# Kernel optimization log

Measured on AMD Instinct MI355X. Metric: run time of the kernel, lower is better.

Reference implementation:

```python
import jax, jax.numpy as jnp
import numpy as np

N = 524288   # sparse points
C = 64       # io channels
AC = 128     # attn channels
H = 8        # heads
PS = 64      # patch size
HID = 256    # mlp hidden (mlp_ratio=2)
HD = AC // H # head dim
EPS = 1e-5


def _ln(x):
    mu = x.mean(-1, keepdims=True)
    v = x.var(-1, keepdims=True)
    return (x - mu) / jnp.sqrt(v + EPS)


def setup_inputs() -> dict:
    key = jax.random.key(0)
    ks = jax.random.split(key, 12)
    def w(k, shape, fan_in):
        return jax.random.normal(k, shape, jnp.float32) * (1.0 / np.sqrt(fan_in))
    return {
        "feats": jax.random.normal(ks[0], (N, C), jnp.float32),
        "w_pre": w(ks[1], (C, AC), C),    "b_pre": jnp.zeros((AC,), jnp.float32),
        "g1": jnp.ones((AC,), jnp.float32), "b1": jnp.zeros((AC,), jnp.float32),
        "w_qkv": w(ks[2], (AC, 3 * AC), AC), "b_qkv": jnp.zeros((3 * AC,), jnp.float32),
        "w_proj": w(ks[3], (AC, AC), AC), "b_proj": jnp.zeros((AC,), jnp.float32),
        "g2": jnp.ones((AC,), jnp.float32), "b2": jnp.zeros((AC,), jnp.float32),
        "w_m1": w(ks[4], (AC, HID), AC),  "b_m1": jnp.zeros((HID,), jnp.float32),
        "w_m2": w(ks[5], (HID, AC), HID), "b_m2": jnp.zeros((AC,), jnp.float32),
        "w_post": w(ks[6], (AC, C), AC),  "b_post": jnp.zeros((C,), jnp.float32),
    }


def reference(feats, w_pre, b_pre, g1, b1, w_qkv, b_qkv, w_proj, b_proj,
              g2, b2, w_m1, b_m1, w_m2, b_m2, w_post, b_post):
    # pre_proj: 1x1 sparse conv == pointwise linear on [N, C]
    x2 = feats @ w_pre + b_pre                            # [N, AC]
    # norm1 -> patch attention
    n1 = _ln(x2) * g1 + b1
    P = N // PS
    qkv = (n1 @ w_qkv + b_qkv).reshape(P, PS, 3, H, HD)   # patches of 64 pts
    q, k, v = qkv[:, :, 0], qkv[:, :, 1], qkv[:, :, 2]    # [P, PS, H, HD]
    scale = HD ** -0.5
    att = jnp.einsum('pqhd,pkhd->phqk', q, k) * scale     # [P, H, PS, PS]
    att = jax.nn.softmax(att, axis=-1)
    o = jnp.einsum('phqk,pkhd->pqhd', att, v).reshape(N, AC)
    h = o @ w_proj + b_proj
    x2 = x2 + h                                           # residual 1
    # norm2 -> pointwise MLP (1x1 conv -> GELU -> 1x1 conv)
    n2 = _ln(x2) * g2 + b2
    h2 = jax.nn.gelu(n2 @ w_m1 + b_m1, approximate=False) @ w_m2 + b_m2
    x2 = x2 + h2                                          # residual 2
    return x2 @ w_post + b_post                           # post_proj [N, C]
```

## Files before the change

### kernel.cpp

```cpp
#include <hip/hip_runtime.h>
#include <hip/hip_bf16.h>
#include <math.h>


typedef __bf16 bf16;
typedef __bf16 bf16x8 __attribute__((ext_vector_type(8)));
typedef __bf16 bf16x4 __attribute__((ext_vector_type(4)));
typedef float  f32x4  __attribute__((ext_vector_type(4)));

#define MFMA16(a, b, c) __builtin_amdgcn_mfma_f32_16x16x32_bf16((a), (b), (c), 0, 0, 0)

constexpr int OFF_PRE  = 0;
constexpr int OFF_QKV  = 8192;
constexpr int OFF_PROJ = 57344;
constexpr int OFF_M1   = 73728;
constexpr int OFF_M2   = 106496;
constexpr int OFF_POST = 139264;

template <int W>
__device__ __forceinline__ int swz(int row, int col) {
    constexpr int CH = W >> 3;
    constexpr int M  = (CH - 1) < 15 ? (CH - 1) : 15;
    const int c = (col >> 3) ^ (row & M);
    return row * W + c * 8 + (col & 7);
}

__device__ __forceinline__ bf16x8 zero8() {
    bf16x8 z;
#pragma unroll
    for (int j = 0; j < 8; ++j) z[j] = (bf16)0.0f;
    return z;
}

__device__ __forceinline__ void st4(bf16* p, const f32x4 v) {
    bf16x4 o;
#pragma unroll
    for (int r = 0; r < 4; ++r) o[r] = (bf16)v[r];
    *(bf16x4*)p = o;
}

__device__ __forceinline__ float gelu_f(float x) {
    const float u = 0.79788456f * x * (1.0f + 0.044715f * x * x);
    const float e = __builtin_amdgcn_exp2f(u * 2.8853900817779268f);
    return x - x * __builtin_amdgcn_rcpf(e + 1.0f);
}

__global__ void pack_all(const float* __restrict__ w_pre,
                         const float* __restrict__ w_qkv,
                         const float* __restrict__ w_proj,
                         const float* __restrict__ w_m1,
                         const float* __restrict__ w_m2,
                         const float* __restrict__ w_post,
                         bf16* __restrict__ dst) {
    const int t = blockIdx.x;
    const float* src;
    int Ncol, KT, off, t0;
    if (t < 16)       { src = w_pre;  Ncol = 128; KT = 2; off = OFF_PRE;  t0 = 0; }
    else if (t < 112) { src = w_qkv;  Ncol = 384; KT = 4; off = OFF_QKV;  t0 = 16; }
    else if (t < 144) { src = w_proj; Ncol = 128; KT = 4; off = OFF_PROJ; t0 = 112; }
    else if (t < 208) { src = w_m1;   Ncol = 256; KT = 4; off = OFF_M1;   t0 = 144; }
    else if (t < 272) { src = w_m2;   Ncol = 128; KT = 8; off = OFF_M2;   t0 = 208; }
    else              { src = w_post; Ncol = 64;  KT = 4; off = OFF_POST; t0 = 272; }
    const int tile = t - t0;
    const int lane = threadIdx.x;
    const int mt = tile / KT, kt = tile - mt * KT;
    const int n  = mt * 16 + (lane & 15);
    const int k0 = kt * 32 + (lane >> 4) * 8;
    bf16x8 v;
#pragma unroll
    for (int j = 0; j < 8; ++j) v[j] = (bf16)src[(k0 + j) * Ncol + n];
    *(bf16x8*)(dst + off + ((long)(tile * 64 + lane)) * 8) = v;
}

__device__ __forceinline__ void ln_rows(const bf16* __restrict__ in,
                                        bf16* __restrict__ outb,
                                        const float* __restrict__ g,
                                        const float* __restrict__ b, int tid) {
    const int row = tid >> 3, sub = tid & 7;
    bf16x8 c0 = *(const bf16x8*)(in + swz<128>(row, sub * 16));
    bf16x8 c1 = *(const bf16x8*)(in + swz<128>(row, sub * 16 + 8));
    float v[16];
#pragma unroll
    for (int j = 0; j < 8; ++j) { v[j] = (float)c0[j]; v[8 + j] = (float)c1[j]; }
    float s = 0.f, ss = 0.f;
#pragma unroll
    for (int j = 0; j < 16; ++j) { s += v[j]; ss += v[j] * v[j]; }
#pragma unroll
    for (int m = 1; m <= 4; m <<= 1) {
        s += __shfl_xor(s, m);
        ss += __shfl_xor(ss, m);
    }
    const float mu   = s * (1.0f / 128.0f);
    const float rstd = __builtin_amdgcn_rsqf(ss * (1.0f / 128.0f) - mu * mu + 1e-5f);
    bf16x8 o0, o1;
#pragma unroll
    for (int j = 0; j < 8; ++j) {
        o0[j] = (bf16)((v[j] - mu) * rstd * g[sub * 16 + j] + b[sub * 16 + j]);
        o1[j] = (bf16)((v[8 + j] - mu) * rstd * g[sub * 16 + 8 + j] + b[sub * 16 + 8 + j]);
    }
    *(bf16x8*)(outb + swz<128>(row, sub * 16)) = o0;
    *(bf16x8*)(outb + swz<128>(row, sub * 16 + 8)) = o1;
}

__global__ __launch_bounds__(512, 4)
void fused_block_kernel(const float* __restrict__ feats,
                        const bf16* __restrict__ wp,
                        const float* __restrict__ b_pre,
                        const float* __restrict__ g1, const float* __restrict__ b1,
                        const float* __restrict__ b_qkv,
                        const float* __restrict__ b_proj,
                        const float* __restrict__ g2, const float* __restrict__ b2,
                        const float* __restrict__ b_m1,
                        const float* __restrict__ b_m2,
                        const float* __restrict__ b_post,
                        float* __restrict__ out) {
    __shared__ __align__(16) bf16 R1[64 * 128];
    __shared__ __align__(16) bf16 R2[64 * 128];
    __shared__ __align__(16) bf16 R34[64 * 256];
    bf16* const R3 = R34;
    bf16* const R4 = R34 + 64 * 128;

    const int tid  = threadIdx.x;
    const int w    = tid >> 6;
    const int lane = tid & 63;
    const int q    = lane >> 4;
    const int l15  = lane & 15;
    const long base = (long)blockIdx.x * 64;
    const f32x4 fzero = {0.f, 0.f, 0.f, 0.f};

    {
        const int row = tid >> 3, ch = tid & 7;
        const float* src = feats + (base + row) * 64 + ch * 8;
        float4 a = *(const float4*)src;
        float4 b = *(const float4*)(src + 4);
        bf16x8 v;
        v[0] = (bf16)a.x; v[1] = (bf16)a.y; v[2] = (bf16)a.z; v[3] = (bf16)a.w;
        v[4] = (bf16)b.x; v[5] = (bf16)b.y; v[6] = (bf16)b.z; v[7] = (bf16)b.w;
        *(bf16x8*)(R2 + swz<64>(row, ch * 8)) = v;
    }
    __syncthreads();

    f32x4 x2[4];

    {
        f32x4 acc[4];
#pragma unroll
        for (int tt = 0; tt < 4; ++tt) acc[tt] = fzero;
#pragma unroll
        for (int ks = 0; ks < 2; ++ks) {
            bf16x8 afr = *(const bf16x8*)(wp + OFF_PRE + ((w * 2 + ks) * 64 + lane) * 8);
#pragma unroll
            for (int tt = 0; tt < 4; ++tt) {
                bf16x8 bfr = *(const bf16x8*)(R2 + swz<64>(tt * 16 + l15, ks * 32 + q * 8));
                acc[tt] = MFMA16(afr, bfr, acc[tt]);
            }
        }
        const f32x4 bias = *(const f32x4*)(b_pre + w * 16 + q * 4);
#pragma unroll
        for (int tt = 0; tt < 4; ++tt) {
#pragma unroll
            for (int r = 0; r < 4; ++r) x2[tt][r] = acc[tt][r] + bias[r];
            st4(R3 + swz<128>(tt * 16 + l15, w * 16 + q * 4), x2[tt]);
        }
    }
    __syncthreads();

    ln_rows(R3, R1, g1, b1, tid);
    __syncthreads();

    {
        bf16x8 B[4][4];
#pragma unroll
        for (int ks = 0; ks < 4; ++ks)
#pragma unroll
            for (int tt = 0; tt < 4; ++tt)
                B[ks][tt] = *(const bf16x8*)(R1 + swz<128>(tt * 16 + l15, ks * 32 + q * 8));
#pragma unroll
        for (int part = 0; part < 3; ++part) {
            const int mt = part * 8 + w;
            f32x4 acc[4];
#pragma unroll
            for (int tt = 0; tt < 4; ++tt) acc[tt] = fzero;
#pragma unroll
            for (int ks = 0; ks < 4; ++ks) {
                bf16x8 afr = *(const bf16x8*)(wp + OFF_QKV + ((mt * 4 + ks) * 64 + lane) * 8);
#pragma unroll
                for (int tt = 0; tt < 4; ++tt) acc[tt] = MFMA16(afr, B[ks][tt], acc[tt]);
            }
            const f32x4 bias = *(const f32x4*)(b_qkv + mt * 16 + q * 4);
            if (part == 0) {
#pragma unroll
                for (int tt = 0; tt < 4; ++tt)
                    st4(R2 + swz<128>(tt * 16 + l15, w * 16 + q * 4), acc[tt] + bias);
            } else if (part == 1) {
#pragma unroll
                for (int tt = 0; tt < 4; ++tt)
                    st4(R3 + swz<128>(tt * 16 + l15, w * 16 + q * 4), acc[tt] + bias);
            } else {
#pragma unroll
                for (int tt = 0; tt < 4; ++tt)
#pragma unroll
                    for (int r = 0; r < 4; ++r)
                        R4[w * 1024 + swz<64>(q * 4 + r, tt * 16 + l15)] =
                            (bf16)(acc[tt][r] + bias[r]);
            }
        }
    }
    __syncthreads();

    {
        const int colA = w * 16 + (q & 1) * 8;
        const bool hi = (q >= 2);
        const bf16x8 z8 = zero8();
        bf16x8 Kf[4];
#pragma unroll
        for (int kt = 0; kt < 4; ++kt) {
            bf16x8 t = *(const bf16x8*)(R3 + swz<128>(kt * 16 + l15, colA));
            Kf[kt] = hi ? z8 : t;
        }
#pragma unroll
        for (int qt = 0; qt < 4; ++qt) {
            bf16x8 t = *(const bf16x8*)(R2 + swz<128>(qt * 16 + l15, colA));
            bf16x8 Qf = hi ? z8 : t;
            f32x4 S[4];
#pragma unroll
            for (int kt = 0; kt < 4; ++kt) S[kt] = MFMA16(Kf[kt], Qf, fzero);
            float P[4][4];
            float mx = -1e30f;
#pragma unroll
            for (int kt = 0; kt < 4; ++kt)
#pragma unroll
                for (int r = 0; r < 4; ++r) {
                    const float sv = S[kt][r] * 0.25f;
                    P[kt][r] = sv;
                    mx = fmaxf(mx, sv);
                }
            mx = fmaxf(mx, __shfl_xor(mx, 16));
            mx = fmaxf(mx, __shfl_xor(mx, 32));
            float lsum = 0.f;
#pragma unroll
            for (int kt = 0; kt < 4; ++kt)
#pragma unroll
                for (int r = 0; r < 4; ++r) {
                    const float e = __builtin_amdgcn_exp2f((P[kt][r] - mx) * 1.4426950408889634f);
                    P[kt][r] = e;
                    lsum += e;
                }
            lsum += __shfl_xor(lsum, 16);
            lsum += __shfl_xor(lsum, 32);
            const float inv = __builtin_amdgcn_rcpf(lsum);
#pragma unroll
            for (int kt = 0; kt < 4; ++kt)
#pragma unroll
                for (int r = 0; r < 4; ++r) P[kt][r] *= inv;
            f32x4 O = fzero;
#pragma unroll
            for (int ks = 0; ks < 2; ++ks) {
                bf16x8 Bf;
#pragma unroll
                for (int j = 0; j < 8; ++j) {
                    const int src = (((q & 1) * 2 + (j >> 2)) << 4) + l15;
                    const float v0 = __shfl(P[ks * 2][j & 3], src);
                    const float v1 = __shfl(P[ks * 2 + 1][j & 3], src);
                    Bf[j] = (bf16)((q >> 1) ? v1 : v0);
                }
                bf16x8 Af = *(const bf16x8*)(R4 + w * 1024 + swz<64>(l15, ks * 32 + q * 8));
                O = MFMA16(Af, Bf, O);
            }
            st4(R1 + swz<128>(qt * 16 + l15, w * 16 + q * 4), O);
        }
    }
    __syncthreads();

    {
        f32x4 acc[4];
#pragma unroll
        for (int tt = 0; tt < 4; ++tt) acc[tt] = fzero;
#pragma unroll
        for (int ks = 0; ks < 4; ++ks) {
            bf16x8 afr = *(const bf16x8*)(wp + OFF_PROJ + ((w * 4 + ks) * 64 + lane) * 8);
#pragma unroll
            for (int tt = 0; tt < 4; ++tt) {
                bf16x8 bfr = *(const bf16x8*)(R1 + swz<128>(tt * 16 + l15, ks * 32 + q * 8));
                acc[tt] = MFMA16(afr, bfr, acc[tt]);
            }
        }
        const f32x4 bias = *(const f32x4*)(b_proj + w * 16 + q * 4);
#pragma unroll
        for (int tt = 0; tt < 4; ++tt) {
#pragma unroll
            for (int r = 0; r < 4; ++r) x2[tt][r] += acc[tt][r] + bias[r];
            st4(R3 + swz<128>(tt * 16 + l15, w * 16 + q * 4), x2[tt]);
        }
    }
    __syncthreads();

    ln_rows(R3, R1, g2, b2, tid);
    __syncthreads();

    {
        bf16x8 B[4][4];
#pragma unroll
        for (int ks = 0; ks < 4; ++ks)
#pragma unroll
            for (int tt = 0; tt < 4; ++tt)
                B[ks][tt] = *(const bf16x8*)(R1 + swz<128>(tt * 16 + l15, ks * 32 + q * 8));
#pragma unroll
        for (int half = 0; half < 2; ++half) {
            const int mt = w * 2 + half;
            f32x4 acc[4];
#pragma unroll
            for (int tt = 0; tt < 4; ++tt) acc[tt] = fzero;
#pragma unroll
            for (int ks = 0; ks < 4; ++ks) {
                bf16x8 afr = *(const bf16x8*)(wp + OFF_M1 + ((mt * 4 + ks) * 64 + lane) * 8);
#pragma unroll
                for (int tt = 0; tt < 4; ++tt) acc[tt] = MFMA16(afr, B[ks][tt], acc[tt]);
            }
            const f32x4 bias = *(const f32x4*)(b_m1 + mt * 16 + q * 4);
#pragma unroll
            for (int tt = 0; tt < 4; ++tt) {
                f32x4 gl;
#pragma unroll
                for (int r = 0; r < 4; ++r) gl[r] = gelu_f(acc[tt][r] + bias[r]);
                st4(R34 + swz<256>(tt * 16 + l15, mt * 16 + q * 4), gl);
            }
        }
    }
    __syncthreads();

    {
        f32x4 acc[4];
#pragma unroll
        for (int tt = 0; tt < 4; ++tt) acc[tt] = fzero;
#pragma unroll
        for (int ks = 0; ks < 8; ++ks) {
            bf16x8 afr = *(const bf16x8*)(wp + OFF_M2 + ((w * 8 + ks) * 64 + lane) * 8);
#pragma unroll
            for (int tt = 0; tt < 4; ++tt) {
                bf16x8 bfr = *(const bf16x8*)(R34 + swz<256>(tt * 16 + l15, ks * 32 + q * 8));
                acc[tt] = MFMA16(afr, bfr, acc[tt]);
            }
        }
        const f32x4 bias = *(const f32x4*)(b_m2 + w * 16 + q * 4);
#pragma unroll
        for (int tt = 0; tt < 4; ++tt) {
#pragma unroll
            for (int r = 0; r < 4; ++r) x2[tt][r] += acc[tt][r] + bias[r];
            st4(R1 + swz<128>(tt * 16 + l15, w * 16 + q * 4), x2[tt]);
        }
    }
    __syncthreads();

    {
        const int ct  = w >> 1;
        const int tt0 = (w & 1) * 2;
        f32x4 acc[2];
#pragma unroll
        for (int rr = 0; rr < 2; ++rr) acc[rr] = fzero;
#pragma unroll
        for (int ks = 0; ks < 4; ++ks) {
            bf16x8 afr = *(const bf16x8*)(wp + OFF_POST + ((ct * 4 + ks) * 64 + lane) * 8);
#pragma unroll
            for (int rr = 0; rr < 2; ++rr) {
                bf16x8 bfr = *(const bf16x8*)(R1 + swz<128>((tt0 + rr) * 16 + l15, ks * 32 + q * 8));
                acc[rr] = MFMA16(afr, bfr, acc[rr]);
            }
        }
        const f32x4 bias = *(const f32x4*)(b_post + ct * 16 + q * 4);
#pragma unroll
        for (int rr = 0; rr < 2; ++rr) {
            f32x4 v = acc[rr] + bias;
            *(f32x4*)(out + (base + (tt0 + rr) * 16 + l15) * 64 + ct * 16 + q * 4) = v;
        }
    }
}

extern "C" void kernel_launch(void* const* d_in, const int* in_sizes, int n_in,
                              void* d_out, int out_size, void* d_ws, size_t ws_size,
                              hipStream_t stream) {
    const float* feats  = (const float*)d_in[0];
    const float* w_pre  = (const float*)d_in[1];
    const float* b_pre  = (const float*)d_in[2];
    const float* g1     = (const float*)d_in[3];
    const float* b1     = (const float*)d_in[4];
    const float* w_qkv  = (const float*)d_in[5];
    const float* b_qkv  = (const float*)d_in[6];
    const float* w_proj = (const float*)d_in[7];
    const float* b_proj = (const float*)d_in[8];
    const float* g2     = (const float*)d_in[9];
    const float* b2     = (const float*)d_in[10];
    const float* w_m1   = (const float*)d_in[11];
    const float* b_m1   = (const float*)d_in[12];
    const float* w_m2   = (const float*)d_in[13];
    const float* b_m2   = (const float*)d_in[14];
    const float* w_post = (const float*)d_in[15];
    const float* b_post = (const float*)d_in[16];

    bf16* wp = (bf16*)d_ws;

    pack_all<<<288, 64, 0, stream>>>(w_pre, w_qkv, w_proj, w_m1, w_m2, w_post, wp);

    fused_block_kernel<<<8192, 512, 0, stream>>>(
        feats, wp, b_pre, g1, b1, b_qkv, b_proj, g2, b2, b_m1, b_m2, b_post,
        (float*)d_out);
}
```

Measured before the change: 634.5 us.

## Shrink shared memory to three 16KB buffers and route softmax probs through LDS

Cuts LDS from 64KB to 48KB per block by aliasing buffers: Q goes into the LN output buffer (an extra barrier protects the reads), and the MLP hidden activations are split across two 128-wide buffers. The launch-bounds occupancy hint rises from 4 to 6 blocks. The attention P->B-fragment transpose now goes through a per-wave LDS slab instead of 16 cross-lane shuffles, and V fragments are loaded once per wave. The costs are an extra barrier, LDS round trips for P, and more register pressure under the higher occupancy target.

After: 1.315 ms. +107.3%, slower.

```diff
diff --git a/kernel.cpp b/kernel.cpp
--- a/kernel.cpp
+++ b/kernel.cpp
@@ -102,7 +102,7 @@
     *(bf16x8*)(outb + swz<128>(row, sub * 16 + 8)) = o1;
 }
 
-__global__ __launch_bounds__(512, 4)
+__global__ __launch_bounds__(512, 6)
 void fused_block_kernel(const float* __restrict__ feats,
                         const bf16* __restrict__ wp,
                         const float* __restrict__ b_pre,
@@ -114,11 +114,9 @@
                         const float* __restrict__ b_m2,
                         const float* __restrict__ b_post,
                         float* __restrict__ out) {
-    __shared__ __align__(16) bf16 R1[64 * 128];
-    __shared__ __align__(16) bf16 R2[64 * 128];
-    __shared__ __align__(16) bf16 R34[64 * 256];
-    bf16* const R3 = R34;
-    bf16* const R4 = R34 + 64 * 128;
+    __shared__ __align__(16) bf16 RA[64 * 128];
+    __shared__ __align__(16) bf16 RB[64 * 128];
+    __shared__ __align__(16) bf16 RC[64 * 128];
 
     const int tid  = threadIdx.x;
     const int w    = tid >> 6;
@@ -136,7 +134,7 @@
         bf16x8 v;
         v[0] = (bf16)a.x; v[1] = (bf16)a.y; v[2] = (bf16)a.z; v[3] = (bf16)a.w;
         v[4] = (bf16)b.x; v[5] = (bf16)b.y; v[6] = (bf16)b.z; v[7] = (bf16)b.w;
-        *(bf16x8*)(R2 + swz<64>(row, ch * 8)) = v;
+        *(bf16x8*)(RA + swz<64>(row, ch * 8)) = v;
     }
     __syncthreads();
 
@@ -151,7 +149,7 @@
             bf16x8 afr = *(const bf16x8*)(wp + OFF_PRE + ((w * 2 + ks) * 64 + lane) * 8);
 #pragma unroll
             for (int tt = 0; tt < 4; ++tt) {
-                bf16x8 bfr = *(const bf16x8*)(R2 + swz<64>(tt * 16 + l15, ks * 32 + q * 8));
+                bf16x8 bfr = *(const bf16x8*)(RA + swz<64>(tt * 16 + l15, ks * 32 + q * 8));
                 acc[tt] = MFMA16(afr, bfr, acc[tt]);
             }
         }
@@ -160,21 +158,22 @@
         for (int tt = 0; tt < 4; ++tt) {
 #pragma unroll
             for (int r = 0; r < 4; ++r) x2[tt][r] = acc[tt][r] + bias[r];
-            st4(R3 + swz<128>(tt * 16 + l15, w * 16 + q * 4), x2[tt]);
-        }
-    }
-    __syncthreads();
-
-    ln_rows(R3, R1, g1, b1, tid);
-    __syncthreads();
-
-    {
-        bf16x8 B[4][4];
+            st4(RB + swz<128>(tt * 16 + l15, w * 16 + q * 4), x2[tt]);
+        }
+    }
+    __syncthreads();
+
+    ln_rows(RB, RA, g1, b1, tid);
+    __syncthreads();
+
+    {
+        bf16x8 Bfr[4][4];
 #pragma unroll
         for (int ks = 0; ks < 4; ++ks)
 #pragma unroll
             for (int tt = 0; tt < 4; ++tt)
-                B[ks][tt] = *(const bf16x8*)(R1 + swz<128>(tt * 16 + l15, ks * 32 + q * 8));
+                Bfr[ks][tt] = *(const bf16x8*)(RA + swz<128>(tt * 16 + l15, ks * 32 + q * 8));
+        __syncthreads();
 #pragma unroll
         for (int part = 0; part < 3; ++part) {
             const int mt = part * 8 + w;
@@ -185,23 +184,23 @@
             for (int ks = 0; ks < 4; ++ks) {
                 bf16x8 afr = *(const bf16x8*)(wp + OFF_QKV + ((mt * 4 + ks) * 64 + lane) * 8);
 #pragma unroll
-                for (int tt = 0; tt < 4; ++tt) acc[tt] = MFMA16(afr, B[ks][tt], acc[tt]);
+                for (int tt = 0; tt < 4; ++tt) acc[tt] = MFMA16(afr, Bfr[ks][tt], acc[tt]);
             }
             const f32x4 bias = *(const f32x4*)(b_qkv + mt * 16 + q * 4);
             if (part == 0) {
 #pragma unroll
                 for (int tt = 0; tt < 4; ++tt)
-                    st4(R2 + swz<128>(tt * 16 + l15, w * 16 + q * 4), acc[tt] + bias);
+                    st4(RA + swz<128>(tt * 16 + l15, w * 16 + q * 4), acc[tt] + bias);
             } else if (part == 1) {
 #pragma unroll
                 for (int tt = 0; tt < 4; ++tt)
-                    st4(R3 + swz<128>(tt * 16 + l15, w * 16 + q * 4), acc[tt] + bias);
+                    st4(RB + swz<128>(tt * 16 + l15, w * 16 + q * 4), acc[tt] + bias);
             } else {
 #pragma unroll
                 for (int tt = 0; tt < 4; ++tt)
 #pragma unroll
                     for (int r = 0; r < 4; ++r)
-                        R4[w * 1024 + swz<64>(q * 4 + r, tt * 16 + l15)] =
+                        RC[w * 1024 + swz<64>(q * 4 + r, tt * 16 + l15)] =
                             (bf16)(acc[tt][r] + bias[r]);
             }
         }
@@ -212,15 +211,20 @@
         const int colA = w * 16 + (q & 1) * 8;
         const bool hi = (q >= 2);
         const bf16x8 z8 = zero8();
+        bf16* const slab = RC + w * 1024;
         bf16x8 Kf[4];
 #pragma unroll
         for (int kt = 0; kt < 4; ++kt) {
-            bf16x8 t = *(const bf16x8*)(R3 + swz<128>(kt * 16 + l15, colA));
+            bf16x8 t = *(const bf16x8*)(RB + swz<128>(kt * 16 + l15, colA));
             Kf[kt] = hi ? z8 : t;
         }
+        bf16x8 Vf[2];
+#pragma unroll
+        for (int ks = 0; ks < 2; ++ks)
+            Vf[ks] = *(const bf16x8*)(slab + swz<64>(l15, ks * 32 + q * 8));
 #pragma unroll
         for (int qt = 0; qt < 4; ++qt) {
-            bf16x8 t = *(const bf16x8*)(R2 + swz<128>(qt * 16 + l15, colA));
+            bf16x8 t = *(const bf16x8*)(RA + swz<128>(qt * 16 + l15, colA));
             bf16x8 Qf = hi ? z8 : t;
             f32x4 S[4];
 #pragma unroll
@@ -250,24 +254,19 @@
             lsum += __shfl_xor(lsum, 32);
             const float inv = __builtin_amdgcn_rcpf(lsum);
 #pragma unroll
-            for (int kt = 0; kt < 4; ++kt)
-#pragma unroll
-                for (int r = 0; r < 4; ++r) P[kt][r] *= inv;
+            for (int kt = 0; kt < 4; ++kt) {
+                f32x4 e4;
+#pragma unroll
+                for (int r = 0; r < 4; ++r) e4[r] = P[kt][r] * inv;
+                st4(slab + swz<64>(l15, kt * 16 + q * 4), e4);
+            }
             f32x4 O = fzero;
 #pragma unroll
             for (int ks = 0; ks < 2; ++ks) {
-                bf16x8 Bf;
-#pragma unroll
-                for (int j = 0; j < 8; ++j) {
-                    const int src = (((q & 1) * 2 + (j >> 2)) << 4) + l15;
-                    const float v0 = __shfl(P[ks * 2][j & 3], src);
-                    const float v1 = __shfl(P[ks * 2 + 1][j & 3], src);
-                    Bf[j] = (bf16)((q >> 1) ? v1 : v0);
-                }
-                bf16x8 Af = *(const bf16x8*)(R4 + w * 1024 + swz<64>(l15, ks * 32 + q * 8));
-                O = MFMA16(Af, Bf, O);
-            }
-            st4(R1 + swz<128>(qt * 16 + l15, w * 16 + q * 4), O);
+                bf16x8 Bf = *(const bf16x8*)(slab + swz<64>(l15, ks * 32 + q * 8));
+                O = MFMA16(Vf[ks], Bf, O);
+            }
+            st4(RA + swz<128>(qt * 16 + l15, w * 16 + q * 4), O);
         }
     }
     __syncthreads();
@@ -281,7 +280,7 @@
             bf16x8 afr = *(const bf16x8*)(wp + OFF_PROJ + ((w * 4 + ks) * 64 + lane) * 8);
 #pragma unroll
             for (int tt = 0; tt < 4; ++tt) {
-                bf16x8 bfr = *(const bf16x8*)(R1 + swz<128>(tt * 16 + l15, ks * 32 + q * 8));
+                bf16x8 bfr = *(const bf16x8*)(RA + swz<128>(tt * 16 + l15, ks * 32 + q * 8));
                 acc[tt] = MFMA16(afr, bfr, acc[tt]);
             }
         }
@@ -290,21 +289,21 @@
         for (int tt = 0; tt < 4; ++tt) {
 #pragma unroll
             for (int r = 0; r < 4; ++r) x2[tt][r] += acc[tt][r] + bias[r];
-            st4(R3 + swz<128>(tt * 16 + l15, w * 16 + q * 4), x2[tt]);
-        }
-    }
-    __syncthreads();
-
-    ln_rows(R3, R1, g2, b2, tid);
-    __syncthreads();
-
-    {
-        bf16x8 B[4][4];
+            st4(RB + swz<128>(tt * 16 + l15, w * 16 + q * 4), x2[tt]);
+        }
+    }
+    __syncthreads();
+
+    ln_rows(RB, RA, g2, b2, tid);
+    __syncthreads();
+
+    {
+        bf16x8 Bfr[4][4];
 #pragma unroll
         for (int ks = 0; ks < 4; ++ks)
 #pragma unroll
             for (int tt = 0; tt < 4; ++tt)
-                B[ks][tt] = *(const bf16x8*)(R1 + swz<128>(tt * 16 + l15, ks * 32 + q * 8));
+                Bfr[ks][tt] = *(const bf16x8*)(RA + swz<128>(tt * 16 + l15, ks * 32 + q * 8));
 #pragma unroll
         for (int half = 0; half < 2; ++half) {
             const int mt = w * 2 + half;
@@ -315,15 +314,17 @@
             for (int ks = 0; ks < 4; ++ks) {
                 bf16x8 afr = *(const bf16x8*)(wp + OFF_M1 + ((mt * 4 + ks) * 64 + lane) * 8);
 #pragma unroll
-                for (int tt = 0; tt < 4; ++tt) acc[tt] = MFMA16(afr, B[ks][tt], acc[tt]);
+                for (int tt = 0; tt < 4; ++tt) acc[tt] = MFMA16(afr, Bfr[ks][tt], acc[tt]);
             }
             const f32x4 bias = *(const f32x4*)(b_m1 + mt * 16 + q * 4);
+            bf16* const dst = (mt < 8) ? RB : RC;
+            const int colb  = (mt & 7) * 16 + q * 4;
 #pragma unroll
             for (int tt = 0; tt < 4; ++tt) {
                 f32x4 gl;
 #pragma unroll
                 for (int r = 0; r < 4; ++r) gl[r] = gelu_f(acc[tt][r] + bias[r]);
-                st4(R34 + swz<256>(tt * 16 + l15, mt * 16 + q * 4), gl);
+                st4(dst + swz<128>(tt * 16 + l15, colb), gl);
             }
         }
     }
@@ -336,9 +337,11 @@
 #pragma unroll
         for (int ks = 0; ks < 8; ++ks) {
             bf16x8 afr = *(const bf16x8*)(wp + OFF_M2 + ((w * 8 + ks) * 64 + lane) * 8);
+            const bf16* const srcH = (ks < 4) ? RB : RC;
+            const int colb = (ks & 3) * 32 + q * 8;
 #pragma unroll
             for (int tt = 0; tt < 4; ++tt) {
-                bf16x8 bfr = *(const bf16x8*)(R34 + swz<256>(tt * 16 + l15, ks * 32 + q * 8));
+                bf16x8 bfr = *(const bf16x8*)(srcH + swz<128>(tt * 16 + l15, colb));
                 acc[tt] = MFMA16(afr, bfr, acc[tt]);
             }
         }
@@ -347,7 +350,7 @@
         for (int tt = 0; tt < 4; ++tt) {
 #pragma unroll
             for (int r = 0; r < 4; ++r) x2[tt][r] += acc[tt][r] + bias[r];
-            st4(R1 + swz<128>(tt * 16 + l15, w * 16 + q * 4), x2[tt]);
+            st4(RA + swz<128>(tt * 16 + l15, w * 16 + q * 4), x2[tt]);
         }
     }
     __syncthreads();
@@ -363,7 +366,7 @@
             bf16x8 afr = *(const bf16x8*)(wp + OFF_POST + ((ct * 4 + ks) * 64 + lane) * 8);
 #pragma unroll
             for (int rr = 0; rr < 2; ++rr) {
-                bf16x8 bfr = *(const bf16x8*)(R1 + swz<128>((tt0 + rr) * 16 + l15, ks * 32 + q * 8));
+                bf16x8 bfr = *(const bf16x8*)(RA + swz<128>((tt0 + rr) * 16 + l15, ks * 32 + q * 8));
                 acc[rr] = MFMA16(afr, bfr, acc[rr]);
             }
         }
```
